# Performance work log

Hardware: AMD Instinct MI355X
Metric: run time of the kernel (lower is better)

Reference implementation:

```python
import jax, jax.numpy as jnp
import numpy as np

TEMPERATURE = 0.07
HARD_NEG_RATIO = 0.5
B, D, N_CLASSES = 2048, 512, 100


def setup_inputs() -> dict:
    key = jax.random.key(0)
    kf, kl = jax.random.split(key)
    features = jax.random.normal(kf, (B, D), dtype=jnp.float32)
    # L2-normalize as is standard for SupCon embeddings (keeps logits well-scaled)
    features = features / jnp.linalg.norm(features, axis=1, keepdims=True)
    labels = jax.random.randint(kl, (B,), 0, N_CLASSES, dtype=jnp.int64)
    return {"features": features, "labels": labels}


def reference(features, labels):
    b = features.shape[0]
    dt = features.dtype
    lab = labels.reshape(-1, 1)
    mask = (lab == lab.T).astype(dt)                       # [B,B] positives (incl. self)
    adc = (features @ features.T) / TEMPERATURE            # [B,B] logits
    logits_max = jax.lax.stop_gradient(jnp.max(adc, axis=1, keepdims=True))
    logits = adc - logits_max                              # row-stabilized
    logits_mask = 1.0 - jnp.eye(b, dtype=dt)               # exclude self
    negative_mask = (1.0 - mask) * logits_mask
    neg_b = negative_mask > 0

    # top-k hard-negative threshold: k-th largest negative logit (global over all pairs).
    # k is data-dependent, so use a full descending sort + dynamic gather (jit-safe).
    flat = jnp.where(neg_b, logits, -jnp.inf).ravel()      # [B*B]
    sorted_desc = -jnp.sort(-flat)
    n_neg = jnp.sum(neg_b)
    k = jnp.maximum(1, (HARD_NEG_RATIO * n_neg).astype(jnp.int32))  # floor, >=1
    threshold = sorted_desc[k - 1]
    hard_negatives_mask = ((logits >= threshold) & neg_b).astype(dt)

    final_mask = jnp.minimum(mask + hard_negatives_mask, 1.0) * logits_mask
    row_pos = final_mask.sum(axis=1)
    single_samples = (row_pos == 0).astype(dt)

    exp_logits = jnp.exp(logits) * logits_mask
    log_prob = logits - jnp.log(exp_logits.sum(axis=1, keepdims=True) + 1e-12)
    mean_log_prob_pos = (final_mask * log_prob).sum(axis=1) / (row_pos + single_samples)
    loss_vec = -mean_log_prob_pos * (1.0 - single_samples)
    loss = loss_vec.sum() / (b - single_samples.sum())
    return (loss, hard_negatives_mask, final_mask)
```

## Files before the change

### kernel.cpp

```cpp
#include <hip/hip_runtime.h>
#include <cstddef>

constexpr int Bn   = 2048;
constexpr int Dn   = 512;
constexpr int NCLS = 100;
constexpr int CAP  = 131072;
constexpr unsigned WWIN = 32768;


struct Ctl {
  unsigned above;
  unsigned candCount;
  unsigned singles;
  unsigned done;
  float    thrF;
  unsigned pad1;
  double   lossSum;
  unsigned hist[4096];
  unsigned cand[CAP];
};
static_assert(offsetof(Ctl, cand) % 16 == 0, "cand must be 16B aligned");

__device__ inline unsigned key_of(float L) {
  unsigned u = __float_as_uint(L);
  return (u & 0x80000000u) ? ~u : (u | 0x80000000u);
}
__device__ inline float key_to_float(unsigned key) {
  unsigned u = (key & 0x80000000u) ? (key ^ 0x80000000u) : ~key;
  return __uint_as_float(u);
}
__device__ inline unsigned wlo_key() {
  const float c0 = -1.0f / 0.07f;
  return key_of(c0) - (WWIN / 2);
}
__device__ inline void store16_a4(float* p, float4 v) {
  __builtin_memcpy((void*)p, &v, 16);
}

__global__ __launch_bounds__(256) void rowdot_k(const float* __restrict__ F,
                                                float* __restrict__ rm) {
  const int i = blockIdx.x * 256 + threadIdx.x;
  const float4* p = (const float4*)(F + (size_t)i * Dn);
  float acc = 0.0f;
#pragma unroll 16
  for (int q = 0; q < 128; ++q) {
    const float4 f = p[q];
    acc = __builtin_fmaf(f.x, f.x, acc);
    acc = __builtin_fmaf(f.y, f.y, acc);
    acc = __builtin_fmaf(f.z, f.z, acc);
    acc = __builtin_fmaf(f.w, f.w, acc);
  }
  rm[i] = acc / 0.07f;
}

__global__ __launch_bounds__(256) void gemm_adc(const float* __restrict__ F,
                                                const float* __restrict__ rm,
                                                const int* __restrict__ labels,
                                                float* __restrict__ adc, Ctl* c) {
  __shared__ float smem[4352];
  __shared__ int slabi[64], slabj[64];
  __shared__ float rmiA[64], rmjA[64];
  __shared__ unsigned wlist[1024];
  __shared__ unsigned wcnt, abcnt, gbase;
  const int t = threadIdx.x;
  int r = 0;
  { const int idx = blockIdx.x; while ((r + 1) * (r + 2) / 2 <= idx) ++r; }
  const int cc = blockIdx.x - r * (r + 1) / 2;
  const int i0 = r * 64, j0 = cc * 64;

  const int tx = t & 15, ty = t >> 4;
  const int lrow = t >> 2, lq = t & 3;

  if (t < 64) {
    slabi[t] = labels[i0 + t]; rmiA[t] = rm[i0 + t];
    slabj[t] = labels[j0 + t]; rmjA[t] = rm[j0 + t];
  }
  if (t == 0) { wcnt = 0; abcnt = 0; gbase = 0; }

  float acc[4][4] = {};
  const float* Ab = F + (size_t)(i0 + lrow) * Dn;
  const float* Bb = F + (size_t)(j0 + lrow) * Dn;
  float* As = smem;
  float* Bs = smem + 2176;

  float4 a = *(const float4*)(Ab + lq * 4);
  float4 b = *(const float4*)(Bb + lq * 4);
  {
    const int k0 = lq * 4;
    As[(k0 + 0) * 68 + lrow] = a.x; As[(k0 + 1) * 68 + lrow] = a.y;
    As[(k0 + 2) * 68 + lrow] = a.z; As[(k0 + 3) * 68 + lrow] = a.w;
    Bs[(k0 + 0) * 68 + lrow] = b.x; Bs[(k0 + 1) * 68 + lrow] = b.y;
    Bs[(k0 + 2) * 68 + lrow] = b.z; Bs[(k0 + 3) * 68 + lrow] = b.w;
  }
  __syncthreads();

  for (int ch = 0; ch < 32; ++ch) {
    const int cur = ch & 1, nxt = cur ^ 1;
    if (ch < 31) {
      const int kg = (ch + 1) * 16;
      a = *(const float4*)(Ab + kg + lq * 4);
      b = *(const float4*)(Bb + kg + lq * 4);
    }
    const float* Ac = As + cur * 1088;
    const float* Bc = Bs + cur * 1088;
#pragma unroll
    for (int k = 0; k < 16; ++k) {
      const float4 av = *(const float4*)(Ac + k * 68 + ty * 4);
      const float4 bv = *(const float4*)(Bc + k * 68 + tx * 4);
      const float aa[4] = {av.x, av.y, av.z, av.w};
      const float bb[4] = {bv.x, bv.y, bv.z, bv.w};
#pragma unroll
      for (int m = 0; m < 4; ++m)
#pragma unroll
        for (int n = 0; n < 4; ++n)
          acc[m][n] = __builtin_fmaf(aa[m], bb[n], acc[m][n]);
    }
    if (ch < 31) {
      const int k0 = lq * 4;
      float* An = As + nxt * 1088;
      float* Bm = Bs + nxt * 1088;
      An[(k0 + 0) * 68 + lrow] = a.x; An[(k0 + 1) * 68 + lrow] = a.y;
      An[(k0 + 2) * 68 + lrow] = a.z; An[(k0 + 3) * 68 + lrow] = a.w;
      Bm[(k0 + 0) * 68 + lrow] = b.x; Bm[(k0 + 1) * 68 + lrow] = b.y;
      Bm[(k0 + 2) * 68 + lrow] = b.z; Bm[(k0 + 3) * 68 + lrow] = b.w;
    }
    __syncthreads();
  }

  float v[4][4];
#pragma unroll
  for (int m = 0; m < 4; ++m) {
#pragma unroll
    for (int n = 0; n < 4; ++n) v[m][n] = acc[m][n] / 0.07f;
    float4 q = {v[m][0], v[m][1], v[m][2], v[m][3]};
    *(float4*)&adc[(size_t)(i0 + ty * 4 + m) * Bn + j0 + tx * 4] = q;
  }
  if (r != cc) {
    __syncthreads();
    float* T = smem;
#pragma unroll
    for (int m = 0; m < 4; ++m)
#pragma unroll
      for (int n = 0; n < 4; ++n)
        T[(tx * 4 + n) * 68 + (ty * 4 + m)] = v[m][n];
    __syncthreads();
#pragma unroll
    for (int e = 0; e < 4; ++e) {
      const int row2 = e * 16 + ty;
      *(float4*)&adc[(size_t)(j0 + row2) * Bn + i0 + tx * 4] =
          *(const float4*)(T + row2 * 68 + tx * 4);
    }
  }

  __syncthreads();
  const unsigned klo = wlo_key(), khi = klo + WWIN;
  unsigned myab = 0;
#pragma unroll
  for (int m = 0; m < 4; ++m) {
    const int gi = i0 + ty * 4 + m;
    const int li = slabi[ty * 4 + m];
    const float rmi = rmiA[ty * 4 + m];
#pragma unroll
    for (int n = 0; n < 4; ++n) {
      const int gj = j0 + tx * 4 + n;
      if (gi == gj || li == slabj[tx * 4 + n]) continue;
      const unsigned key = key_of(v[m][n] - rmi);
      if (key >= khi) ++myab;
      else if (key >= klo) {
        atomicAdd(&c->hist[(key - klo) >> 3], 1u);
        const unsigned p = atomicAdd(&wcnt, 1u);
        if (p < 1024u) wlist[p] = key;
      }
      if (r != cc) {
        const unsigned key2 = key_of(v[m][n] - rmjA[tx * 4 + n]);
        if (key2 >= khi) ++myab;
        else if (key2 >= klo) {
          atomicAdd(&c->hist[(key2 - klo) >> 3], 1u);
          const unsigned p = atomicAdd(&wcnt, 1u);
          if (p < 1024u) wlist[p] = key2;
        }
      }
    }
  }
  if (myab) atomicAdd(&abcnt, myab);
  __syncthreads();
  if (t == 0) {
    if (abcnt) atomicAdd(&c->above, abcnt);
    const unsigned nl = wcnt < 1024u ? wcnt : 1024u;
    gbase = nl ? atomicAdd(&c->candCount, nl) : 0u;
  }
  __syncthreads();
  const unsigned nl = wcnt < 1024u ? wcnt : 1024u;
  for (unsigned q = t; q < nl; q += 256) {
    const unsigned p = gbase + q;
    if (p < (unsigned)CAP) c->cand[p] = wlist[q];
  }
}

__global__ __launch_bounds__(256) void select_k(const int* __restrict__ labels, Ctl* c) {
  __shared__ unsigned cnt[NCLS];
  __shared__ unsigned tsum[256], suffix[256];
  __shared__ unsigned skk;
  __shared__ int sbd;
  __shared__ unsigned sab, m;
  __shared__ unsigned list[256];
  const int t = threadIdx.x;
  if (t < NCLS) cnt[t] = 0;
  if (t == 0) { m = 0; sbd = 0; sab = 0; }
  __syncthreads();
  for (int j = t; j < Bn; j += 256) atomicAdd(&cnt[labels[j]], 1u);
  __syncthreads();
  if (t == 0) {
    unsigned s = 0;
    for (int h = 0; h < NCLS; ++h) s += cnt[h] * cnt[h];
    unsigned nneg = (unsigned)Bn * Bn - s;
    unsigned k = nneg >> 1;
    if (k < 1) k = 1;
    skk = k;
  }
  const uint4* hp = (const uint4*)c->hist;
  uint4 h0 = hp[t * 4 + 0], h1 = hp[t * 4 + 1], h2 = hp[t * 4 + 2], h3 = hp[t * 4 + 3];
  const unsigned hv[16] = {h0.x, h0.y, h0.z, h0.w, h1.x, h1.y, h1.z, h1.w,
                           h2.x, h2.y, h2.z, h2.w, h3.x, h3.y, h3.z, h3.w};
  unsigned s = 0;
#pragma unroll
  for (int u = 0; u < 16; ++u) s += hv[u];
  tsum[t] = s;
  __syncthreads();
  if (t == 0) {
    unsigned acc = c->above;
    for (int q = 255; q >= 0; --q) { suffix[q] = acc; acc += tsum[q]; }
  }
  __syncthreads();
  const unsigned kk = skk;
  unsigned cum = suffix[t];
#pragma unroll
  for (int u = 15; u >= 0; --u) {
    if (cum < kk && cum + hv[u] >= kk) { sbd = t * 16 + u; sab = cum; }
    cum += hv[u];
  }
  __syncthreads();
  const int bd = sbd;
  const unsigned rr = kk - sab;
  const unsigned klo = wlo_key();
  unsigned n = c->candCount; if (n > (unsigned)CAP) n = (unsigned)CAP;
  const unsigned n4 = n >> 2;
  const uint4* cp = (const uint4*)c->cand;
  unsigned q = t;
  for (; q + 7u * 256u < n4; q += 8u * 256u) {
    uint4 v[8];
#pragma unroll
    for (int u = 0; u < 8; ++u) v[u] = cp[q + (unsigned)u * 256u];
#pragma unroll
    for (int u = 0; u < 8; ++u) {
      const unsigned ks[4] = {v[u].x, v[u].y, v[u].z, v[u].w};
#pragma unroll
      for (int w = 0; w < 4; ++w) {
        const unsigned d = ks[w] - klo;
        if (d < WWIN && (int)(d >> 3) == bd) {
          const unsigned p = atomicAdd(&m, 1u);
          if (p < 256u) list[p] = ks[w];
        }
      }
    }
  }
  for (; q < n4; q += 256u) {
    const uint4 v = cp[q];
    const unsigned ks[4] = {v.x, v.y, v.z, v.w};
#pragma unroll
    for (int w = 0; w < 4; ++w) {
      const unsigned d = ks[w] - klo;
      if (d < WWIN && (int)(d >> 3) == bd) {
        const unsigned p = atomicAdd(&m, 1u);
        if (p < 256u) list[p] = ks[w];
      }
    }
  }
  for (unsigned e = n4 * 4u + t; e < n; e += 256u) {
    const unsigned key = c->cand[e];
    const unsigned d = key - klo;
    if (d < WWIN && (int)(d >> 3) == bd) {
      const unsigned p = atomicAdd(&m, 1u);
      if (p < 256u) list[p] = key;
    }
  }
  __syncthreads();
  const unsigned mm = m > 256u ? 256u : m;
  for (unsigned e = t; e < mm; e += 256) {
    const unsigned v = list[e];
    unsigned g = 0, ge = 0;
    for (unsigned j = 0; j < mm; ++j) {
      g  += (list[j] > v);
      ge += (list[j] >= v);
    }
    if (g < rr && rr <= ge) c->thrF = key_to_float(v);
  }
}

__global__ __launch_bounds__(256) void final_k(const float* __restrict__ adc,
                                               const int* __restrict__ labels,
                                               Ctl* c, float* __restrict__ out) {
  __shared__ int slab[Bn];
  __shared__ double lsum[8];
  __shared__ unsigned sflag[8];
  const int t = threadIdx.x;
  const int lane = t & 63, w = t >> 6;
#pragma unroll
  for (int e = 0; e < 2; ++e)
    ((int4*)slab)[t + 256 * e] = ((const int4*)labels)[t + 256 * e];
  __syncthreads();
  const float thr = c->thrF;
  float* __restrict__ ohnm = out + 1;
  float* __restrict__ ofin = out + 1 + (size_t)Bn * Bn;

#pragma unroll
  for (int rr = 0; rr < 2; ++rr) {
    const int i = blockIdx.x * 8 + rr * 4 + w;
    const int li = slab[i];
    const float rm = adc[(size_t)i * Bn + i];
    const float4* rowp = (const float4*)(adc + (size_t)i * Bn);
    float se = 0.0f, sp = 0.0f;
    int pc = 0;
#pragma unroll
    for (int q = 0; q < 8; ++q) {
      const int j4 = lane + 64 * q;
      const float4 vv = rowp[j4];
      const int jb = j4 * 4;
      const float vs[4] = {vv.x, vv.y, vv.z, vv.w};
      float qh[4], qf[4];
#pragma unroll
      for (int u = 0; u < 4; ++u) {
        const int j = jb + u;
        const float L = vs[u] - rm;
        const bool offd = (j != i);
        const bool same = (slab[j] == li);
        const bool hnm  = offd && !same && (L >= thr);
        const bool fin  = offd && (same || hnm);
        if (offd) se += __expf(L);
        if (fin)  { sp += L; ++pc; }
        qh[u] = hnm ? 1.0f : 0.0f;
        qf[u] = fin ? 1.0f : 0.0f;
      }
      float4 h4 = {qh[0], qh[1], qh[2], qh[3]};
      float4 f4 = {qf[0], qf[1], qf[2], qf[3]};
      store16_a4(&ohnm[(size_t)i * Bn + jb], h4);
      store16_a4(&ofin[(size_t)i * Bn + jb], f4);
    }
    float pcf = (float)pc;
#pragma unroll
    for (int o = 32; o > 0; o >>= 1) {
      se  += __shfl_down(se,  o, 64);
      sp  += __shfl_down(sp,  o, 64);
      pcf += __shfl_down(pcf, o, 64);
    }
    if (lane == 0) {
      const double P = (double)pcf;
      const bool single = (P == 0.0);
      const double mlpp = ((double)sp - P * log((double)se + 1e-12)) / (P + (single ? 1.0 : 0.0));
      lsum[w * 2 + rr]  = single ? 0.0 : -mlpp;
      sflag[w * 2 + rr] = single ? 1u : 0u;
    }
  }
  __syncthreads();
  if (t == 0) {
    double ls = 0.0;
    unsigned sc = 0;
    for (int e = 0; e < 8; ++e) { ls += lsum[e]; sc += sflag[e]; }
    atomicAdd(&c->lossSum, ls);
    if (sc) atomicAdd(&c->singles, sc);
    __threadfence();
    const unsigned ticket = atomicAdd(&c->done, 1u);
    if (ticket == 255u) {
      const double tot = atomicAdd(&c->lossSum, 0.0);
      const unsigned sg = atomicAdd(&c->singles, 0u);
      out[0] = (float)(tot / ((double)Bn - (double)sg));
    }
  }
}

extern "C" void kernel_launch(void* const* d_in, const int* in_sizes, int n_in,
                              void* d_out, int out_size, void* d_ws, size_t ws_size,
                              hipStream_t stream) {
  const float* F      = (const float*)d_in[0];
  const int*   labels = (const int*)d_in[1];
  float* out = (float*)d_out;

  char* ws = (char*)d_ws;
  Ctl*   c   = (Ctl*)ws;
  float* rm  = (float*)(ws + 786432);
  float* adc = (float*)(ws + (1u << 20));

  hipMemsetAsync(c, 0, offsetof(Ctl, cand), stream);

  rowdot_k<<<Bn / 256, 256, 0, stream>>>(F, rm);
  gemm_adc<<<528, 256, 0, stream>>>(F, rm, labels, adc, c);
  select_k<<<1, 256, 0, stream>>>(labels, c);
  final_k<<<256, 256, 0, stream>>>(adc, labels, c, out);
}
```

Before: 182.3 us.

## Split GEMM tiles into half-row blocks, fold memset into rowdot, widen final grid

Each triangular 64x64 tile of the Gram matrix is now handled by two blocks of 32 rows, doubling gemm_adc's grid so the 256 compute units get more work. The final kernel now processes one row per wave instead of two per wave, again doubling the grid. The separate hipMemsetAsync of the control header is replaced by a zeroing loop in rowdot_k, removing one launch. In exchange, the B tile is loaded twice as often, each thread has less register reuse, and half the threads idle while A is loaded.

```diff
diff --git a/kernel.cpp b/kernel.cpp
--- a/kernel.cpp
+++ b/kernel.cpp
@@ -20,6 +20,7 @@
   unsigned cand[CAP];
 };
 static_assert(offsetof(Ctl, cand) % 16 == 0, "cand must be 16B aligned");
+static_assert(offsetof(Ctl, cand) == 16416, "zeroed head size");
 
 __device__ inline unsigned key_of(float L) {
   unsigned u = __float_as_uint(L);
@@ -38,7 +39,7 @@
 }
 
 __global__ __launch_bounds__(256) void rowdot_k(const float* __restrict__ F,
-                                                float* __restrict__ rm) {
+                                                float* __restrict__ rm, Ctl* c) {
   const int i = blockIdx.x * 256 + threadIdx.x;
   const float4* p = (const float4*)(F + (size_t)i * Dn);
   float acc = 0.0f;
@@ -51,46 +52,50 @@
     acc = __builtin_fmaf(f.w, f.w, acc);
   }
   rm[i] = acc / 0.07f;
+  unsigned* cz = (unsigned*)c;
+  for (int idx = i; idx < 4104; idx += 2048) cz[idx] = 0;
 }
 
 __global__ __launch_bounds__(256) void gemm_adc(const float* __restrict__ F,
                                                 const float* __restrict__ rm,
                                                 const int* __restrict__ labels,
                                                 float* __restrict__ adc, Ctl* c) {
-  __shared__ float smem[4352];
-  __shared__ int slabi[64], slabj[64];
-  __shared__ float rmiA[64], rmjA[64];
+  __shared__ float smem[3264];
+  __shared__ int slabi[32], slabj[64];
+  __shared__ float rmiA[32], rmjA[64];
   __shared__ unsigned wlist[1024];
   __shared__ unsigned wcnt, abcnt, gbase;
   const int t = threadIdx.x;
+  const int tile = blockIdx.x >> 1, h = blockIdx.x & 1;
   int r = 0;
-  { const int idx = blockIdx.x; while ((r + 1) * (r + 2) / 2 <= idx) ++r; }
-  const int cc = blockIdx.x - r * (r + 1) / 2;
-  const int i0 = r * 64, j0 = cc * 64;
+  { while ((r + 1) * (r + 2) / 2 <= tile) ++r; }
+  const int cc = tile - r * (r + 1) / 2;
+  const int i0 = r * 64 + h * 32, j0 = cc * 64;
 
   const int tx = t & 15, ty = t >> 4;
   const int lrow = t >> 2, lq = t & 3;
 
-  if (t < 64) {
-    slabi[t] = labels[i0 + t]; rmiA[t] = rm[i0 + t];
-    slabj[t] = labels[j0 + t]; rmjA[t] = rm[j0 + t];
-  }
+  if (t < 32) { slabi[t] = labels[i0 + t]; rmiA[t] = rm[i0 + t]; }
+  if (t < 64) { slabj[t] = labels[j0 + t]; rmjA[t] = rm[j0 + t]; }
   if (t == 0) { wcnt = 0; abcnt = 0; gbase = 0; }
 
-  float acc[4][4] = {};
+  float acc[2][4] = {};
   const float* Ab = F + (size_t)(i0 + lrow) * Dn;
   const float* Bb = F + (size_t)(j0 + lrow) * Dn;
   float* As = smem;
-  float* Bs = smem + 2176;
-
-  float4 a = *(const float4*)(Ab + lq * 4);
+  float* Bs = smem + 1088;
+
+  float4 a = {0.f, 0.f, 0.f, 0.f};
   float4 b = *(const float4*)(Bb + lq * 4);
+  if (t < 128) a = *(const float4*)(Ab + lq * 4);
   {
     const int k0 = lq * 4;
-    As[(k0 + 0) * 68 + lrow] = a.x; As[(k0 + 1) * 68 + lrow] = a.y;
-    As[(k0 + 2) * 68 + lrow] = a.z; As[(k0 + 3) * 68 + lrow] = a.w;
     Bs[(k0 + 0) * 68 + lrow] = b.x; Bs[(k0 + 1) * 68 + lrow] = b.y;
     Bs[(k0 + 2) * 68 + lrow] = b.z; Bs[(k0 + 3) * 68 + lrow] = b.w;
+    if (t < 128) {
+      As[(k0 + 0) * 34 + lrow] = a.x; As[(k0 + 1) * 34 + lrow] = a.y;
+      As[(k0 + 2) * 34 + lrow] = a.z; As[(k0 + 3) * 34 + lrow] = a.w;
+    }
   }
   __syncthreads();
 
@@ -98,57 +103,60 @@
     const int cur = ch & 1, nxt = cur ^ 1;
     if (ch < 31) {
       const int kg = (ch + 1) * 16;
-      a = *(const float4*)(Ab + kg + lq * 4);
       b = *(const float4*)(Bb + kg + lq * 4);
-    }
-    const float* Ac = As + cur * 1088;
+      if (t < 128) a = *(const float4*)(Ab + kg + lq * 4);
+    }
+    const float* Ac = As + cur * 544;
     const float* Bc = Bs + cur * 1088;
 #pragma unroll
     for (int k = 0; k < 16; ++k) {
-      const float4 av = *(const float4*)(Ac + k * 68 + ty * 4);
+      const float2 av = *(const float2*)(Ac + k * 34 + ty * 2);
       const float4 bv = *(const float4*)(Bc + k * 68 + tx * 4);
-      const float aa[4] = {av.x, av.y, av.z, av.w};
+      const float aa[2] = {av.x, av.y};
       const float bb[4] = {bv.x, bv.y, bv.z, bv.w};
 #pragma unroll
-      for (int m = 0; m < 4; ++m)
+      for (int m = 0; m < 2; ++m)
 #pragma unroll
         for (int n = 0; n < 4; ++n)
           acc[m][n] = __builtin_fmaf(aa[m], bb[n], acc[m][n]);
     }
     if (ch < 31) {
       const int k0 = lq * 4;
-      float* An = As + nxt * 1088;
       float* Bm = Bs + nxt * 1088;
-      An[(k0 + 0) * 68 + lrow] = a.x; An[(k0 + 1) * 68 + lrow] = a.y;
-      An[(k0 + 2) * 68 + lrow] = a.z; An[(k0 + 3) * 68 + lrow] = a.w;
       Bm[(k0 + 0) * 68 + lrow] = b.x; Bm[(k0 + 1) * 68 + lrow] = b.y;
       Bm[(k0 + 2) * 68 + lrow] = b.z; Bm[(k0 + 3) * 68 + lrow] = b.w;
+      if (t < 128) {
+        float* An = As + nxt * 544;
+        An[(k0 + 0) * 34 + lrow] = a.x; An[(k0 + 1) * 34 + lrow] = a.y;
+        An[(k0 + 2) * 34 + lrow] = a.z; An[(k0 + 3) * 34 + lrow] = a.w;
+      }
     }
     __syncthreads();
   }
 
-  float v[4][4];
-#pragma unroll
-  for (int m = 0; m < 4; ++m) {
+  float v[2][4];
+#pragma unroll
+  for (int m = 0; m < 2; ++m) {
 #pragma unroll
     for (int n = 0; n < 4; ++n) v[m][n] = acc[m][n] / 0.07f;
     float4 q = {v[m][0], v[m][1], v[m][2], v[m][3]};
-    *(float4*)&adc[(size_t)(i0 + ty * 4 + m) * Bn + j0 + tx * 4] = q;
+    *(float4*)&adc[(size_t)(i0 + ty * 2 + m) * Bn + j0 + tx * 4] = q;
   }
   if (r != cc) {
     __syncthreads();
     float* T = smem;
 #pragma unroll
-    for (int m = 0; m < 4; ++m)
+    for (int m = 0; m < 2; ++m)
 #pragma unroll
       for (int n = 0; n < 4; ++n)
-        T[(tx * 4 + n) * 68 + (ty * 4 + m)] = v[m][n];
+        T[(tx * 4 + n) * 36 + (ty * 2 + m)] = v[m][n];
     __syncthreads();
-#pragma unroll
-    for (int e = 0; e < 4; ++e) {
-      const int row2 = e * 16 + ty;
-      *(float4*)&adc[(size_t)(j0 + row2) * Bn + i0 + tx * 4] =
-          *(const float4*)(T + row2 * 68 + tx * 4);
+    const int f = t & 7, rb = t >> 3;
+#pragma unroll
+    for (int e = 0; e < 2; ++e) {
+      const int row2 = e * 32 + rb;
+      *(float4*)&adc[(size_t)(j0 + row2) * Bn + i0 + f * 4] =
+          *(const float4*)(T + row2 * 36 + f * 4);
     }
   }
 
@@ -156,10 +164,10 @@
   const unsigned klo = wlo_key(), khi = klo + WWIN;
   unsigned myab = 0;
 #pragma unroll
-  for (int m = 0; m < 4; ++m) {
-    const int gi = i0 + ty * 4 + m;
-    const int li = slabi[ty * 4 + m];
-    const float rmi = rmiA[ty * 4 + m];
+  for (int m = 0; m < 2; ++m) {
+    const int gi = i0 + ty * 2 + m;
+    const int li = slabi[ty * 2 + m];
+    const float rmi = rmiA[ty * 2 + m];
 #pragma unroll
     for (int n = 0; n < 4; ++n) {
       const int gj = j0 + tx * 4 + n;
@@ -301,8 +309,8 @@
                                                const int* __restrict__ labels,
                                                Ctl* c, float* __restrict__ out) {
   __shared__ int slab[Bn];
-  __shared__ double lsum[8];
-  __shared__ unsigned sflag[8];
+  __shared__ double lsum[4];
+  __shared__ unsigned sflag[4];
   const int t = threadIdx.x;
   const int lane = t & 63, w = t >> 6;
 #pragma unroll
@@ -313,64 +321,61 @@
   float* __restrict__ ohnm = out + 1;
   float* __restrict__ ofin = out + 1 + (size_t)Bn * Bn;
 
-#pragma unroll
-  for (int rr = 0; rr < 2; ++rr) {
-    const int i = blockIdx.x * 8 + rr * 4 + w;
-    const int li = slab[i];
-    const float rm = adc[(size_t)i * Bn + i];
-    const float4* rowp = (const float4*)(adc + (size_t)i * Bn);
-    float se = 0.0f, sp = 0.0f;
-    int pc = 0;
-#pragma unroll
-    for (int q = 0; q < 8; ++q) {
-      const int j4 = lane + 64 * q;
-      const float4 vv = rowp[j4];
-      const int jb = j4 * 4;
-      const float vs[4] = {vv.x, vv.y, vv.z, vv.w};
-      float qh[4], qf[4];
-#pragma unroll
-      for (int u = 0; u < 4; ++u) {
-        const int j = jb + u;
-        const float L = vs[u] - rm;
-        const bool offd = (j != i);
-        const bool same = (slab[j] == li);
-        const bool hnm  = offd && !same && (L >= thr);
-        const bool fin  = offd && (same || hnm);
-        if (offd) se += __expf(L);
-        if (fin)  { sp += L; ++pc; }
-        qh[u] = hnm ? 1.0f : 0.0f;
-        qf[u] = fin ? 1.0f : 0.0f;
-      }
-      float4 h4 = {qh[0], qh[1], qh[2], qh[3]};
-      float4 f4 = {qf[0], qf[1], qf[2], qf[3]};
-      store16_a4(&ohnm[(size_t)i * Bn + jb], h4);
-      store16_a4(&ofin[(size_t)i * Bn + jb], f4);
-    }
-    float pcf = (float)pc;
-#pragma unroll
-    for (int o = 32; o > 0; o >>= 1) {
-      se  += __shfl_down(se,  o, 64);
-      sp  += __shfl_down(sp,  o, 64);
-      pcf += __shfl_down(pcf, o, 64);
-    }
-    if (lane == 0) {
-      const double P = (double)pcf;
-      const bool single = (P == 0.0);
-      const double mlpp = ((double)sp - P * log((double)se + 1e-12)) / (P + (single ? 1.0 : 0.0));
-      lsum[w * 2 + rr]  = single ? 0.0 : -mlpp;
-      sflag[w * 2 + rr] = single ? 1u : 0u;
-    }
+  const int i = blockIdx.x * 4 + w;
+  const int li = slab[i];
+  const float rm = adc[(size_t)i * Bn + i];
+  const float4* rowp = (const float4*)(adc + (size_t)i * Bn);
+  float se = 0.0f, sp = 0.0f;
+  int pc = 0;
+#pragma unroll
+  for (int q = 0; q < 8; ++q) {
+    const int j4 = lane + 64 * q;
+    const float4 vv = rowp[j4];
+    const int jb = j4 * 4;
+    const float vs[4] = {vv.x, vv.y, vv.z, vv.w};
+    float qh[4], qf[4];
+#pragma unroll
+    for (int u = 0; u < 4; ++u) {
+      const int j = jb + u;
+      const float L = vs[u] - rm;
+      const bool offd = (j != i);
+      const bool same = (slab[j] == li);
+      const bool hnm  = offd && !same && (L >= thr);
+      const bool fin  = offd && (same || hnm);
+      if (offd) se += __expf(L);
+      if (fin)  { sp += L; ++pc; }
+      qh[u] = hnm ? 1.0f : 0.0f;
+      qf[u] = fin ? 1.0f : 0.0f;
+    }
+    float4 h4 = {qh[0], qh[1], qh[2], qh[3]};
+    float4 f4 = {qf[0], qf[1], qf[2], qf[3]};
+    store16_a4(&ohnm[(size_t)i * Bn + jb], h4);
+    store16_a4(&ofin[(size_t)i * Bn + jb], f4);
+  }
+  float pcf = (float)pc;
+#pragma unroll
+  for (int o = 32; o > 0; o >>= 1) {
+    se  += __shfl_down(se,  o, 64);
+    sp  += __shfl_down(sp,  o, 64);
+    pcf += __shfl_down(pcf, o, 64);
+  }
+  if (lane == 0) {
+    const double P = (double)pcf;
+    const bool single = (P == 0.0);
+    const double mlpp = ((double)sp - P * log((double)se + 1e-12)) / (P + (single ? 1.0 : 0.0));
+    lsum[w]  = single ? 0.0 : -mlpp;
+    sflag[w] = single ? 1u : 0u;
   }
   __syncthreads();
   if (t == 0) {
     double ls = 0.0;
     unsigned sc = 0;
-    for (int e = 0; e < 8; ++e) { ls += lsum[e]; sc += sflag[e]; }
+    for (int e = 0; e < 4; ++e) { ls += lsum[e]; sc += sflag[e]; }
     atomicAdd(&c->lossSum, ls);
     if (sc) atomicAdd(&c->singles, sc);
     __threadfence();
     const unsigned ticket = atomicAdd(&c->done, 1u);
-    if (ticket == 255u) {
+    if (ticket == 511u) {
       const double tot = atomicAdd(&c->lossSum, 0.0);
       const unsigned sg = atomicAdd(&c->singles, 0u);
       out[0] = (float)(tot / ((double)Bn - (double)sg));
@@ -390,10 +395,8 @@
   float* rm  = (float*)(ws + 786432);
   float* adc = (float*)(ws + (1u << 20));
 
-  hipMemsetAsync(c, 0, offsetof(Ctl, cand), stream);
-
-  rowdot_k<<<Bn / 256, 256, 0, stream>>>(F, rm);
-  gemm_adc<<<528, 256, 0, stream>>>(F, rm, labels, adc, c);
+  rowdot_k<<<Bn / 256, 256, 0, stream>>>(F, rm, c);
+  gemm_adc<<<1056, 256, 0, stream>>>(F, rm, labels, adc, c);
   select_k<<<1, 256, 0, stream>>>(labels, c);
-  final_k<<<256, 256, 0, stream>>>(adc, labels, c, out);
-}
+  final_k<<<512, 256, 0, stream>>>(adc, labels, c, out);
+}
```

After: 196.3 us. 1.08x slower.

## Fold control-block memset into rowdot and replace atomic loss reduction with finalize kernel

Applied to the files above, without the earlier changes.

Removes the hipMemsetAsync by zeroing the control header inside rowdot_k. final_k now handles one row per wave across 512 blocks instead of two rows per wave over 256 blocks. Each block writes its partial loss and singles count to a per-block slot, and a new single-block finalize kernel reduces them, replacing the global atomics and done-ticket scheme. The cost is one extra small kernel launch, paid to drop the memset launch and the atomic contention and to get more parallelism in final_k.

```diff
diff --git a/kernel.cpp b/kernel.cpp
--- a/kernel.cpp
+++ b/kernel.cpp
@@ -20,6 +20,7 @@
   unsigned cand[CAP];
 };
 static_assert(offsetof(Ctl, cand) % 16 == 0, "cand must be 16B aligned");
+static_assert(offsetof(Ctl, cand) == 16416, "zeroed head size");
 
 __device__ inline unsigned key_of(float L) {
   unsigned u = __float_as_uint(L);
@@ -38,7 +39,7 @@
 }
 
 __global__ __launch_bounds__(256) void rowdot_k(const float* __restrict__ F,
-                                                float* __restrict__ rm) {
+                                                float* __restrict__ rm, Ctl* c) {
   const int i = blockIdx.x * 256 + threadIdx.x;
   const float4* p = (const float4*)(F + (size_t)i * Dn);
   float acc = 0.0f;
@@ -51,6 +52,8 @@
     acc = __builtin_fmaf(f.w, f.w, acc);
   }
   rm[i] = acc / 0.07f;
+  unsigned* cz = (unsigned*)c;
+  for (int idx = i; idx < 4104; idx += 2048) cz[idx] = 0;
 }
 
 __global__ __launch_bounds__(256) void gemm_adc(const float* __restrict__ F,
@@ -299,10 +302,13 @@
 
 __global__ __launch_bounds__(256) void final_k(const float* __restrict__ adc,
                                                const int* __restrict__ labels,
-                                               Ctl* c, float* __restrict__ out) {
+                                               const Ctl* __restrict__ c,
+                                               float* __restrict__ out,
+                                               double* __restrict__ lsum_g,
+                                               unsigned* __restrict__ scnt_g) {
   __shared__ int slab[Bn];
-  __shared__ double lsum[8];
-  __shared__ unsigned sflag[8];
+  __shared__ double lsum[4];
+  __shared__ unsigned sflag[4];
   const int t = threadIdx.x;
   const int lane = t & 63, w = t >> 6;
 #pragma unroll
@@ -313,68 +319,78 @@
   float* __restrict__ ohnm = out + 1;
   float* __restrict__ ofin = out + 1 + (size_t)Bn * Bn;
 
-#pragma unroll
-  for (int rr = 0; rr < 2; ++rr) {
-    const int i = blockIdx.x * 8 + rr * 4 + w;
-    const int li = slab[i];
-    const float rm = adc[(size_t)i * Bn + i];
-    const float4* rowp = (const float4*)(adc + (size_t)i * Bn);
-    float se = 0.0f, sp = 0.0f;
-    int pc = 0;
-#pragma unroll
-    for (int q = 0; q < 8; ++q) {
-      const int j4 = lane + 64 * q;
-      const float4 vv = rowp[j4];
-      const int jb = j4 * 4;
-      const float vs[4] = {vv.x, vv.y, vv.z, vv.w};
-      float qh[4], qf[4];
-#pragma unroll
-      for (int u = 0; u < 4; ++u) {
-        const int j = jb + u;
-        const float L = vs[u] - rm;
-        const bool offd = (j != i);
-        const bool same = (slab[j] == li);
-        const bool hnm  = offd && !same && (L >= thr);
-        const bool fin  = offd && (same || hnm);
-        if (offd) se += __expf(L);
-        if (fin)  { sp += L; ++pc; }
-        qh[u] = hnm ? 1.0f : 0.0f;
-        qf[u] = fin ? 1.0f : 0.0f;
-      }
-      float4 h4 = {qh[0], qh[1], qh[2], qh[3]};
-      float4 f4 = {qf[0], qf[1], qf[2], qf[3]};
-      store16_a4(&ohnm[(size_t)i * Bn + jb], h4);
-      store16_a4(&ofin[(size_t)i * Bn + jb], f4);
-    }
-    float pcf = (float)pc;
-#pragma unroll
-    for (int o = 32; o > 0; o >>= 1) {
-      se  += __shfl_down(se,  o, 64);
-      sp  += __shfl_down(sp,  o, 64);
-      pcf += __shfl_down(pcf, o, 64);
-    }
-    if (lane == 0) {
-      const double P = (double)pcf;
-      const bool single = (P == 0.0);
-      const double mlpp = ((double)sp - P * log((double)se + 1e-12)) / (P + (single ? 1.0 : 0.0));
-      lsum[w * 2 + rr]  = single ? 0.0 : -mlpp;
-      sflag[w * 2 + rr] = single ? 1u : 0u;
-    }
+  const int i = blockIdx.x * 4 + w;
+  const int li = slab[i];
+  const float rm = adc[(size_t)i * Bn + i];
+  const float4* rowp = (const float4*)(adc + (size_t)i * Bn);
+  float se = 0.0f, sp = 0.0f;
+  int pc = 0;
+#pragma unroll
+  for (int q = 0; q < 8; ++q) {
+    const int j4 = lane + 64 * q;
+    const float4 vv = rowp[j4];
+    const int jb = j4 * 4;
+    const float vs[4] = {vv.x, vv.y, vv.z, vv.w};
+    float qh[4], qf[4];
+#pragma unroll
+    for (int u = 0; u < 4; ++u) {
+      const int j = jb + u;
+      const float L = vs[u] - rm;
+      const bool offd = (j != i);
+      const bool same = (slab[j] == li);
+      const bool hnm  = offd && !same && (L >= thr);
+      const bool fin  = offd && (same || hnm);
+      if (offd) se += __expf(L);
+      if (fin)  { sp += L; ++pc; }
+      qh[u] = hnm ? 1.0f : 0.0f;
+      qf[u] = fin ? 1.0f : 0.0f;
+    }
+    float4 h4 = {qh[0], qh[1], qh[2], qh[3]};
+    float4 f4 = {qf[0], qf[1], qf[2], qf[3]};
+    store16_a4(&ohnm[(size_t)i * Bn + jb], h4);
+    store16_a4(&ofin[(size_t)i * Bn + jb], f4);
+  }
+  float pcf = (float)pc;
+#pragma unroll
+  for (int o = 32; o > 0; o >>= 1) {
+    se  += __shfl_down(se,  o, 64);
+    sp  += __shfl_down(sp,  o, 64);
+    pcf += __shfl_down(pcf, o, 64);
+  }
+  if (lane == 0) {
+    const double P = (double)pcf;
+    const bool single = (P == 0.0);
+    const double mlpp = ((double)sp - P * log((double)se + 1e-12)) / (P + (single ? 1.0 : 0.0));
+    lsum[w]  = single ? 0.0 : -mlpp;
+    sflag[w] = single ? 1u : 0u;
   }
   __syncthreads();
   if (t == 0) {
-    double ls = 0.0;
-    unsigned sc = 0;
-    for (int e = 0; e < 8; ++e) { ls += lsum[e]; sc += sflag[e]; }
-    atomicAdd(&c->lossSum, ls);
-    if (sc) atomicAdd(&c->singles, sc);
-    __threadfence();
-    const unsigned ticket = atomicAdd(&c->done, 1u);
-    if (ticket == 255u) {
-      const double tot = atomicAdd(&c->lossSum, 0.0);
-      const unsigned sg = atomicAdd(&c->singles, 0u);
-      out[0] = (float)(tot / ((double)Bn - (double)sg));
-    }
+    lsum_g[blockIdx.x] = lsum[0] + lsum[1] + lsum[2] + lsum[3];
+    scnt_g[blockIdx.x] = sflag[0] + sflag[1] + sflag[2] + sflag[3];
+  }
+}
+
+__global__ __launch_bounds__(256) void finalize_k(const double* __restrict__ lsum_g,
+                                                  const unsigned* __restrict__ scnt_g,
+                                                  float* __restrict__ out) {
+  __shared__ double wls[4];
+  __shared__ unsigned wsc[4];
+  const int t = threadIdx.x;
+  const int lane = t & 63, w = t >> 6;
+  double ls = lsum_g[t] + lsum_g[t + 256];
+  unsigned sc = scnt_g[t] + scnt_g[t + 256];
+#pragma unroll
+  for (int o = 32; o > 0; o >>= 1) {
+    ls += __shfl_down(ls, o, 64);
+    sc += __shfl_down(sc, o, 64);
+  }
+  if (lane == 0) { wls[w] = ls; wsc[w] = sc; }
+  __syncthreads();
+  if (t == 0) {
+    const double tot = wls[0] + wls[1] + wls[2] + wls[3];
+    const unsigned sg = wsc[0] + wsc[1] + wsc[2] + wsc[3];
+    out[0] = (float)(tot / ((double)Bn - (double)sg));
   }
 }
 
@@ -386,14 +402,15 @@
   float* out = (float*)d_out;
 
   char* ws = (char*)d_ws;
-  Ctl*   c   = (Ctl*)ws;
-  float* rm  = (float*)(ws + 786432);
-  float* adc = (float*)(ws + (1u << 20));
-
-  hipMemsetAsync(c, 0, offsetof(Ctl, cand), stream);
-
-  rowdot_k<<<Bn / 256, 256, 0, stream>>>(F, rm);
+  Ctl*     c      = (Ctl*)ws;
+  float*   rm     = (float*)(ws + 786432);
+  double*  lsum_g = (double*)(ws + 802816);
+  unsigned* scnt_g = (unsigned*)(ws + 806912);
+  float*   adc    = (float*)(ws + (1u << 20));
+
+  rowdot_k<<<Bn / 256, 256, 0, stream>>>(F, rm, c);
   gemm_adc<<<528, 256, 0, stream>>>(F, rm, labels, adc, c);
   select_k<<<1, 256, 0, stream>>>(labels, c);
-  final_k<<<256, 256, 0, stream>>>(adc, labels, c, out);
-}
+  final_k<<<512, 256, 0, stream>>>(adc, labels, c, out, lsum_g, scnt_g);
+  finalize_k<<<1, 256, 0, stream>>>(lsum_g, scnt_g, out);
+}
```

Result: faster. 173.6 us (-4.8%).
